# Optimization experiments

Measured on AMD Instinct MI355X. Metric: run time of the kernel, lower is better.

The kernel has to match this reference:

```python
import jax, jax.numpy as jnp
import numpy as np

N_NODES = 100000
N_EDGES = 3200000


def setup_inputs() -> dict:
    key = jax.random.key(0)
    k1, k2, k3, k4 = jax.random.split(key, 4)
    x = jax.random.normal(k1, (N_NODES, 16), dtype=jnp.float32)
    edge_index = jax.random.randint(k2, (2, N_EDGES), 0, N_NODES, dtype=jnp.int64)
    # Glorot-ish init like PyG's GCNConv linear layer
    W1 = jax.random.normal(k3, (16, 32), dtype=jnp.float32) * (1.0 / np.sqrt(16))
    b1 = jnp.zeros((32,), dtype=jnp.float32)
    W2 = jax.random.normal(k4, (32, 2), dtype=jnp.float32) * (1.0 / np.sqrt(32))
    b2 = jnp.zeros((2,), dtype=jnp.float32)
    return {"x": x, "edge_index": edge_index, "W1": W1, "b1": b1, "W2": W2, "b2": b2}


def _gcn_conv(x, W, b, src, dst, n):
    """PyG GCNConv: add self-loops, symmetric deg^{-1/2} normalization,
    linear transform, scatter-add aggregation, then bias."""
    h = x @ W  # [N, out]
    ones = jnp.ones(src.shape[0], dtype=x.dtype)
    deg = jax.ops.segment_sum(ones, dst, num_segments=n)  # in-degree incl. self-loops
    dinv = jnp.where(deg > 0, jax.lax.rsqrt(deg), 0.0)
    norm = dinv[src] * dinv[dst]  # [E+N]
    msg = h[src] * norm[:, None]  # gather + scale, [E+N, out]
    out = jax.ops.segment_sum(msg, dst, num_segments=n)  # scatter-add
    return out + b


def reference(x, edge_index, W1, b1, W2, b2):
    n = x.shape[0]
    loop = jnp.arange(n, dtype=edge_index.dtype)
    src = jnp.concatenate([edge_index[0], loop])  # self-loops appended
    dst = jnp.concatenate([edge_index[1], loop])
    h = jax.nn.relu(_gcn_conv(x, W1, b1, src, dst, n))
    return _gcn_conv(h, W2, b2, src, dst, n)
```

## Files before the change

### kernel.cpp

```cpp
#include <hip/hip_runtime.h>
#include <hip/hip_fp16.h>


#define B 256
#define NB_MAX 1024
#define BDIV 128
#define BSHIFT 7
#define CHUNK 4096
#define BCAP 6144
#define RI_MASK 0x7FFFFFu

__global__ __launch_bounds__(256) void k_phist(const int* __restrict__ dst,
                                               unsigned short* __restrict__ hists,
                                               int E, int NB, int NBLK) {
    __shared__ int h[NB_MAX];
    int tid = threadIdx.x, blk = blockIdx.x;
    for (int b = tid; b < NB; b += 256) h[b] = 0;
    __syncthreads();
    int start = blk * CHUNK;
    int end = min(start + CHUNK, E);
    for (int e = start + tid; e < end; e += 256)
        atomicAdd(&h[((unsigned)dst[e]) >> BSHIFT], 1);
    __syncthreads();
    for (int b = tid; b < NB; b += 256) hists[b * NBLK + blk] = (unsigned short)h[b];
}

__global__ __launch_bounds__(1024) void k_pscan1(unsigned short* __restrict__ hists,
                                                 int* __restrict__ totals, int NBLK) {
    __shared__ int s[1024];
    int b = blockIdx.x, tid = threadIdx.x;
    int v = (tid < NBLK) ? (int)hists[b * NBLK + tid] : 0;
    s[tid] = v;
    __syncthreads();
    for (int off = 1; off < 1024; off <<= 1) {
        int u = (tid >= off) ? s[tid - off] : 0;
        __syncthreads();
        s[tid] += u;
        __syncthreads();
    }
    if (tid < NBLK) hists[b * NBLK + tid] = (unsigned short)(s[tid] - v);
    if (tid == 1023) totals[b] = s[1023];
}

__global__ __launch_bounds__(256) void k_move(const int* __restrict__ src,
                                              const int* __restrict__ dst,
                                              const unsigned short* __restrict__ hists,
                                              const int* __restrict__ totals,
                                              unsigned* __restrict__ packed,
                                              int E, int NB, int NBLK) {
    __shared__ unsigned stage[CHUNK];
    __shared__ unsigned short stage_b[CHUNK];
    __shared__ int lh[NB_MAX];
    __shared__ int lexc[NB_MAX];
    __shared__ int gb[NB_MAX];
    __shared__ int part[256];
    int tid = threadIdx.x, blk = blockIdx.x;
    int t4 = tid * 4;
    {
        int a0 = (t4 + 0 < NB) ? totals[t4 + 0] : 0;
        int a1 = (t4 + 1 < NB) ? totals[t4 + 1] : 0;
        int a2 = (t4 + 2 < NB) ? totals[t4 + 2] : 0;
        int a3 = (t4 + 3 < NB) ? totals[t4 + 3] : 0;
        int sum = a0 + a1 + a2 + a3;
        part[tid] = sum;
        __syncthreads();
        for (int off = 1; off < 256; off <<= 1) {
            int u = (tid >= off) ? part[tid - off] : 0;
            __syncthreads();
            part[tid] += u;
            __syncthreads();
        }
        int run = part[tid] - sum;
        if (t4 + 0 < NB) { gb[t4 + 0] = run; run += a0; }
        if (t4 + 1 < NB) { gb[t4 + 1] = run; run += a1; }
        if (t4 + 2 < NB) { gb[t4 + 2] = run; run += a2; }
        if (t4 + 3 < NB) { gb[t4 + 3] = run; run += a3; }
    }
    for (int b = tid; b < NB; b += 256) lh[b] = 0;
    __syncthreads();
    int start = blk * CHUNK;
    int end = min(start + CHUNK, E);
    for (int e = start + tid; e < end; e += 256)
        atomicAdd(&lh[((unsigned)dst[e]) >> BSHIFT], 1);
    __syncthreads();
    {
        int a0 = 0, a1 = 0, a2 = 0, a3 = 0;
        if (t4 + 0 < NB) a0 = lh[t4 + 0];
        if (t4 + 1 < NB) a1 = lh[t4 + 1];
        if (t4 + 2 < NB) a2 = lh[t4 + 2];
        if (t4 + 3 < NB) a3 = lh[t4 + 3];
        int sum = a0 + a1 + a2 + a3;
        part[tid] = sum;
        __syncthreads();
        for (int off = 1; off < 256; off <<= 1) {
            int u = (tid >= off) ? part[tid - off] : 0;
            __syncthreads();
            part[tid] += u;
            __syncthreads();
        }
        int run = part[tid] - sum;
        if (t4 + 0 < NB) { lexc[t4 + 0] = run; run += a0; }
        if (t4 + 1 < NB) { lexc[t4 + 1] = run; run += a1; }
        if (t4 + 2 < NB) { lexc[t4 + 2] = run; run += a2; }
        if (t4 + 3 < NB) { lexc[t4 + 3] = run; run += a3; }
    }
    __syncthreads();
    for (int b = tid; b < NB; b += 256) {
        gb[b] = gb[b] + (int)hists[b * NBLK + blk] - lexc[b];
        lh[b] = lexc[b];
    }
    __syncthreads();
    for (int e = start + tid; e < end; e += 256) {
        unsigned d = (unsigned)dst[e];
        int b = d >> BSHIFT;
        int r = atomicAdd(&lh[b], 1);
        stage[r] = (unsigned)src[e] | ((d & (BDIV - 1u)) << 20);
        stage_b[r] = (unsigned short)b;
    }
    __syncthreads();
    int cnt = end - start;
    for (int i = tid; i < cnt; i += 256)
        packed[gb[stage_b[i]] + i] = stage[i];
}

__global__ __launch_bounds__(256) void k_bucket_csr(const unsigned* __restrict__ packed,
                                                    const int* __restrict__ totals,
                                                    unsigned* __restrict__ rowinfo,
                                                    float* __restrict__ dinv,
                                                    int* __restrict__ col, int n, int NB) {
    __shared__ unsigned stg[BCAP];
    __shared__ int part[256];
    __shared__ int lcnt[BDIV];
    __shared__ int plexc[BDIV];
    __shared__ int sbase[2];
    int b = blockIdx.x, tid = threadIdx.x;
    int t4 = tid * 4;
    {
        int a0 = (t4 + 0 < NB) ? totals[t4 + 0] : 0;
        int a1 = (t4 + 1 < NB) ? totals[t4 + 1] : 0;
        int a2 = (t4 + 2 < NB) ? totals[t4 + 2] : 0;
        int a3 = (t4 + 3 < NB) ? totals[t4 + 3] : 0;
        int sum = a0 + a1 + a2 + a3;
        part[tid] = sum;
        __syncthreads();
        for (int off = 1; off < 256; off <<= 1) {
            int u = (tid >= off) ? part[tid - off] : 0;
            __syncthreads();
            part[tid] += u;
            __syncthreads();
        }
        int run = part[tid] - sum;
        int a[4] = {a0, a1, a2, a3};
#pragma unroll
        for (int q = 0; q < 4; ++q) {
            if (t4 + q == b) { sbase[0] = run; sbase[1] = run + a[q]; }
            run += a[q];
        }
    }
    if (tid < BDIV) lcnt[tid] = 0;
    __syncthreads();
    int s0 = sbase[0], s1 = sbase[1];
    for (int i = s0 + tid; i < s1; i += 256) {
        unsigned u = packed[i];
        int k = i - s0;
        if (k < BCAP) stg[k] = u;
        atomicAdd(&lcnt[u >> 20], 1);
    }
    __syncthreads();
    int v = (tid < BDIV) ? lcnt[tid] : 0;
    int vp = (v + 7) & ~7;
    if (tid < BDIV) plexc[tid] = vp;
    __syncthreads();
    for (int off = 1; off < BDIV; off <<= 1) {
        int u = (tid < BDIV && tid >= off) ? plexc[tid - off] : 0;
        __syncthreads();
        if (tid < BDIV) plexc[tid] += u;
        __syncthreads();
    }
    int cb = s0 + 1024 * b;
    if (tid < BDIV) {
        plexc[tid] -= vp;
        int node = b * BDIV + tid;
        if (node < n) {
            rowinfo[node] = (unsigned)(cb + plexc[tid]) | ((unsigned)(vp >> 3) << 23);
            dinv[node] = rsqrtf((float)(v + 1));
        }
        lcnt[tid] = 0;
    }
    __syncthreads();
    for (int i = s0 + tid; i < s1; i += 256) {
        int k = i - s0;
        unsigned u = (k < BCAP) ? stg[k] : packed[i];
        int l = (int)(u >> 20);
        int pos = cb + plexc[l] + atomicAdd(&lcnt[l], 1);
        col[pos] = (int)(u & 0xFFFFFu);
    }
    __syncthreads();
    if (tid < BDIV) {
        int st = cb + plexc[tid];
        for (int k = v; k < vp; ++k) col[st + k] = n;
    }
}

__global__ void k_prep(const float* __restrict__ x, const float* __restrict__ dinv,
                       __half2* __restrict__ x16, float* __restrict__ t, int n8) {
    int g = blockIdx.x * blockDim.x + threadIdx.x;
    if (g < n8) {
        float d = dinv[g >> 3];
        float2 v = ((const float2*)x)[g];
        x16[g] = __float22half2_rn(make_float2(v.x * d, v.y * d));
    } else if (g < n8 + 8) {
        x16[g] = __float22half2_rn(make_float2(0.f, 0.f));
        if (g == n8) {
            t[(n8 >> 3) * 2 + 0] = 0.f;
            t[(n8 >> 3) * 2 + 1] = 0.f;
        }
    }
}

__global__ __launch_bounds__(256) void k_l1w(const __half2* __restrict__ x16,
                                             const unsigned* __restrict__ rowinfo,
                                             const int* __restrict__ col,
                                             const float* __restrict__ dinv,
                                             float* __restrict__ agg, int n) {
    int tid = threadIdx.x;
    int lane = tid & 63;
    int r = blockIdx.x * 4 + (tid >> 6);
    if (r >= n) return;
    int h = lane & 7, eg = lane >> 3;
    float dr = dinv[r];
    unsigned ri = rowinfo[r];
    int j = (int)(ri & RI_MASK) + eg;
    int trips = (int)(ri >> 23);
    float s0 = 0.f, s1 = 0.f;
    if (eg == 0) {
        float2 f = __half22float2(x16[(size_t)r * 8 + h]);
        s0 = f.x; s1 = f.y;
    }
#pragma unroll 4
    for (int it = 0; it < trips; ++it, j += 8) {
        int sc = col[j];
        float2 f = __half22float2(x16[(size_t)sc * 8 + h]);
        s0 += f.x; s1 += f.y;
    }
    s0 += __shfl_xor(s0, 8);  s1 += __shfl_xor(s1, 8);
    s0 += __shfl_xor(s0, 16); s1 += __shfl_xor(s1, 16);
    s0 += __shfl_xor(s0, 32); s1 += __shfl_xor(s1, 32);
    if (eg == 0)
        *(float2*)(agg + (size_t)r * 16 + 2 * h) = make_float2(s0 * dr, s1 * dr);
}

__global__ __launch_bounds__(256) void k_mlp(const float* __restrict__ agg,
                                             const float* __restrict__ dinv,
                                             const float* __restrict__ W1,
                                             const float* __restrict__ b1,
                                             const float* __restrict__ W2,
                                             float* __restrict__ t, int n) {
    __shared__ float sW1[512], sW2[64], sb1[32];
    int tid = threadIdx.x;
    for (int k = tid; k < 512; k += 256) sW1[k] = W1[k];
    if (tid < 64) sW2[tid] = W2[tid];
    if (tid < 32) sb1[tid] = b1[tid];
    __syncthreads();
    int i = blockIdx.x * 256 + tid;
    if (i >= n) return;
    float a[16];
    const float4* av = (const float4*)(agg + (size_t)i * 16);
#pragma unroll
    for (int q = 0; q < 4; ++q) {
        float4 v = av[q];
        a[4 * q + 0] = v.x; a[4 * q + 1] = v.y;
        a[4 * q + 2] = v.z; a[4 * q + 3] = v.w;
    }
    float di = dinv[i];
    float t0 = 0.f, t1 = 0.f;
#pragma unroll
    for (int j = 0; j < 32; ++j) {
        float acc = sb1[j];
#pragma unroll
        for (int k = 0; k < 16; ++k) acc = fmaf(a[k], sW1[k * 32 + j], acc);
        float hh = fmaxf(acc, 0.f);
        t0 = fmaf(hh, sW2[j * 2 + 0], t0);
        t1 = fmaf(hh, sW2[j * 2 + 1], t1);
    }
    t[(size_t)i * 2 + 0] = t0 * di;
    t[(size_t)i * 2 + 1] = t1 * di;
}

__global__ __launch_bounds__(256) void k_l2w(const unsigned* __restrict__ rowinfo,
                                             const int* __restrict__ col,
                                             const float* __restrict__ dinv,
                                             const float* __restrict__ ts,
                                             const float* __restrict__ b2,
                                             float* __restrict__ out, int n) {
    int g = blockIdx.x * 256 + threadIdx.x;
    int i = g >> 3, q = g & 7;
    if (i >= n) return;
    float di = dinv[i];
    unsigned ri = rowinfo[i];
    int j = (int)(ri & RI_MASK) + q;
    int trips = (int)(ri >> 23);
    float a0 = 0.f, a1 = 0.f;
    if (q == 0) {
        float2 tv = *(const float2*)(ts + (size_t)i * 2);
        a0 = tv.x; a1 = tv.y;
    }
#pragma unroll 4
    for (int it = 0; it < trips; ++it, j += 8) {
        int sc = col[j];
        float2 tv = *(const float2*)(ts + (size_t)sc * 2);
        a0 += tv.x; a1 += tv.y;
    }
    a0 += __shfl_xor(a0, 1); a1 += __shfl_xor(a1, 1);
    a0 += __shfl_xor(a0, 2); a1 += __shfl_xor(a1, 2);
    a0 += __shfl_xor(a0, 4); a1 += __shfl_xor(a1, 4);
    if (q == 0) {
        out[(size_t)i * 2 + 0] = fmaf(a0, di, b2[0]);
        out[(size_t)i * 2 + 1] = fmaf(a1, di, b2[1]);
    }
}


__global__ void k_zero(int* __restrict__ cnt, int n) {
    int i = blockIdx.x * blockDim.x + threadIdx.x;
    if (i < n) cnt[i] = 0;
}
__global__ void k_hist_rank(const int* __restrict__ dst, int* __restrict__ cnt,
                            int* __restrict__ rank, int E) {
    int e = blockIdx.x * blockDim.x + threadIdx.x;
    if (e < E) rank[e] = atomicAdd(&cnt[dst[e]], 1);
}
__global__ __launch_bounds__(256) void k_blocksum(const int* __restrict__ cnt,
                                                  int* __restrict__ bsum, int n) {
    __shared__ int s[256];
    int tid = threadIdx.x;
    int bse = blockIdx.x * 1024 + tid * 4;
    int sum = 0;
#pragma unroll
    for (int q = 0; q < 4; ++q) {
        int i = bse + q;
        if (i < n) sum += (cnt[i] + 7) & ~7;
    }
    s[tid] = sum;
    __syncthreads();
    for (int off = 128; off > 0; off >>= 1) {
        if (tid < off) s[tid] += s[tid + off];
        __syncthreads();
    }
    if (tid == 0) bsum[blockIdx.x] = s[0];
}
__global__ __launch_bounds__(1024) void k_scan_bsums(const int* __restrict__ bsum,
                                                     int* __restrict__ boff, int nb) {
    __shared__ int s[1024];
    int tid = threadIdx.x;
    int v = (tid < nb) ? bsum[tid] : 0;
    s[tid] = v;
    __syncthreads();
    for (int off = 1; off < 1024; off <<= 1) {
        int u = (tid >= off) ? s[tid - off] : 0;
        __syncthreads();
        s[tid] += u;
        __syncthreads();
    }
    if (tid < nb) boff[tid] = s[tid] - v;
}
__global__ __launch_bounds__(256) void k_scan_apply(const int* __restrict__ cnt,
                                                    const int* __restrict__ boff,
                                                    unsigned* __restrict__ rowinfo,
                                                    float* __restrict__ dinv, int n) {
    __shared__ int s[256];
    int tid = threadIdx.x;
    int bse = blockIdx.x * 1024 + tid * 4;
    int c[4];
    int sum = 0;
#pragma unroll
    for (int q = 0; q < 4; ++q) {
        int i = bse + q;
        c[q] = (i < n) ? ((cnt[i] + 7) & ~7) : 0;
        sum += c[q];
    }
    s[tid] = sum;
    __syncthreads();
    for (int off = 1; off < 256; off <<= 1) {
        int u = (tid >= off) ? s[tid - off] : 0;
        __syncthreads();
        s[tid] += u;
        __syncthreads();
    }
    int run = boff[blockIdx.x] + s[tid] - sum;
#pragma unroll
    for (int q = 0; q < 4; ++q) {
        int i = bse + q;
        if (i < n) {
            rowinfo[i] = (unsigned)run | ((unsigned)(c[q] >> 3) << 23);
            run += c[q];
            dinv[i] = rsqrtf((float)(cnt[i] + 1));
        }
    }
}
__global__ void k_fill_rank(const int* __restrict__ src, const int* __restrict__ dst,
                            const unsigned* __restrict__ rowinfo,
                            const int* __restrict__ rank,
                            int* __restrict__ col, int E) {
    int e = blockIdx.x * blockDim.x + threadIdx.x;
    if (e >= E) return;
    int d = dst[e];
    col[(rowinfo[d] & RI_MASK) + rank[e]] = src[e];
}
__global__ void k_pad_sent(const unsigned* __restrict__ rowinfo,
                           const int* __restrict__ cnt,
                           int* __restrict__ col, int n) {
    int i = blockIdx.x * blockDim.x + threadIdx.x;
    if (i >= n) return;
    int st = (int)(rowinfo[i] & RI_MASK);
    int v = cnt[i], vp = (v + 7) & ~7;
    for (int k = v; k < vp; ++k) col[st + k] = n;
}

static inline size_t align4(size_t v) { return (v + 3) & ~(size_t)3; }

extern "C" void kernel_launch(void* const* d_in, const int* in_sizes, int n_in,
                              void* d_out, int out_size, void* d_ws, size_t ws_size,
                              hipStream_t stream) {
    const float* x  = (const float*)d_in[0];
    const int*   ei = (const int*)d_in[1];
    const float* W1 = (const float*)d_in[2];
    const float* b1 = (const float*)d_in[3];
    const float* W2 = (const float*)d_in[4];
    const float* b2 = (const float*)d_in[5];
    float* out = (float*)d_out;

    const int n = in_sizes[0] / 16;
    const int E = in_sizes[1] / 2;
    const int* src = ei;
    const int* dst = ei + E;

    const int gn = (n + B - 1) / B;
    const int ge = (E + B - 1) / B;
    const int n8 = n * 8;

    const int NB   = (n + BDIV - 1) / BDIV;
    const int NBLK = (E + CHUNK - 1) / CHUNK;

    size_t o_hists  = 0;
    size_t o_totals = align4(o_hists + ((size_t)NB * NBLK + 1) / 2);
    size_t o_rowinf = align4(o_totals + NB);
    size_t o_dinv   = align4(o_rowinf + n);
    size_t o_packed = align4(o_dinv + n);
    size_t o_col    = align4(o_packed + E);
    size_t colsz    = (size_t)E + 1024 * (size_t)NB;
    size_t need_r5  = (o_col + colsz) * 4 + 64;
    size_t u_t   = 0;
    size_t u_x16 = align4(2 * (size_t)n + 2);
    size_t u_agg = align4(u_x16 + 8 * (size_t)n + 8);
    size_t reuse_need = u_agg + 16 * (size_t)n;

    bool r5_ok = (NB <= NB_MAX) && (NBLK <= 1024) && (n <= (1 << 20)) &&
                 ((size_t)E + 1024 * (size_t)NB < (RI_MASK + 1)) &&
                 (reuse_need <= (size_t)E) && (ws_size >= need_r5);

    if (r5_ok) {
        int* ws = (int*)d_ws;
        unsigned short* hists = (unsigned short*)(ws + o_hists);
        int*      totals = ws + o_totals;
        unsigned* rowinf = (unsigned*)(ws + o_rowinf);
        float*    dinv   = (float*)(ws + o_dinv);
        unsigned* packed = (unsigned*)(ws + o_packed);
        int*      col    = ws + o_col;
        float*    t      = (float*)(packed + u_t);
        __half2*  x16    = (__half2*)(packed + u_x16);
        float*    agg    = (float*)(packed + u_agg);

        k_phist<<<NBLK, 256, 0, stream>>>(dst, hists, E, NB, NBLK);
        k_pscan1<<<NB, 1024, 0, stream>>>(hists, totals, NBLK);
        k_move<<<NBLK, 256, 0, stream>>>(src, dst, hists, totals, packed, E, NB, NBLK);
        k_bucket_csr<<<NB, 256, 0, stream>>>(packed, totals, rowinf, dinv, col, n, NB);
        k_prep<<<(n8 + 8 + 255) / 256, 256, 0, stream>>>(x, dinv, x16, t, n8);
        k_l1w<<<(n + 3) / 4, 256, 0, stream>>>(x16, rowinf, col, dinv, agg, n);
        k_mlp<<<gn, 256, 0, stream>>>(agg, dinv, W1, b1, W2, t, n);
        k_l2w<<<(8 * n + 255) / 256, 256, 0, stream>>>(rowinf, col, dinv, t, b2, out, n);
        return;
    }

    const int nb = (n + 1023) / 1024;
    size_t f_cnt    = 0;
    size_t f_rowinf = align4(f_cnt + n);
    size_t f_col    = align4(f_rowinf + n);
    size_t f_dinv   = align4(f_col + E + 8 * (size_t)n);
    size_t f_bsum   = align4(f_dinv + n);
    size_t f_boff   = align4(f_bsum + nb);
    size_t f_rank   = align4(f_boff + nb);
    size_t reuse2   = align4(2 * (size_t)n + 2) + align4(8 * (size_t)n + 8) + 16 * (size_t)n;
    size_t rmax = (size_t)E > reuse2 ? (size_t)E : reuse2;
    size_t need_rank = (f_rank + rmax) * 4 + 64;
    if (ws_size >= need_rank && nb <= 1024) {
        int*      ws     = (int*)d_ws;
        int*      cnt    = ws + f_cnt;
        unsigned* rowinf = (unsigned*)(ws + f_rowinf);
        int*      col    = ws + f_col;
        float*    dinv   = (float*)(ws + f_dinv);
        int*      bsum   = ws + f_bsum;
        int*      boff   = ws + f_boff;
        int*      rank   = ws + f_rank;
        float*    t      = (float*)rank;
        __half2*  x16    = (__half2*)(rank + align4(2 * (size_t)n + 2));
        float*    agg    = (float*)(rank + align4(2 * (size_t)n + 2) + align4(8 * (size_t)n + 8));

        k_zero<<<gn, B, 0, stream>>>(cnt, n);
        k_hist_rank<<<ge, B, 0, stream>>>(dst, cnt, rank, E);
        k_blocksum<<<nb, 256, 0, stream>>>(cnt, bsum, n);
        k_scan_bsums<<<1, 1024, 0, stream>>>(bsum, boff, nb);
        k_scan_apply<<<nb, 256, 0, stream>>>(cnt, boff, rowinf, dinv, n);
        k_fill_rank<<<ge, B, 0, stream>>>(src, dst, rowinf, rank, col, E);
        k_pad_sent<<<gn, B, 0, stream>>>(rowinf, cnt, col, n);
        k_prep<<<(n8 + 8 + 255) / 256, 256, 0, stream>>>(x, dinv, x16, t, n8);
        k_l1w<<<(n + 3) / 4, 256, 0, stream>>>(x16, rowinf, col, dinv, agg, n);
        k_mlp<<<gn, 256, 0, stream>>>(agg, dinv, W1, b1, W2, t, n);
        k_l2w<<<(8 * n + 255) / 256, 256, 0, stream>>>(rowinf, col, dinv, t, b2, out, n);
    }
}
```

Baseline: 132.5 us.

## Transpose histogram layout and derive local counts from prefix scan in move kernel

The per-block bucket histogram is stored block-major instead of bucket-major, so the phist writes and the move kernel reads are coalesced. The move kernel no longer re-histograms its chunk of dst. It recovers each block's per-bucket counts as the difference between adjacent blocks' exclusive offsets (or the total for the last block), and fuses the two shared-memory scans into one pass. This removes a full read of dst plus atomics per block, at the cost of strided access in k_pscan1.

```diff
diff --git a/kernel.cpp b/kernel.cpp
--- a/kernel.cpp
+++ b/kernel.cpp
@@ -22,14 +22,16 @@
     for (int e = start + tid; e < end; e += 256)
         atomicAdd(&h[((unsigned)dst[e]) >> BSHIFT], 1);
     __syncthreads();
-    for (int b = tid; b < NB; b += 256) hists[b * NBLK + blk] = (unsigned short)h[b];
+    for (int b = tid; b < NB; b += 256)
+        hists[(size_t)blk * NB + b] = (unsigned short)h[b];
 }
 
 __global__ __launch_bounds__(1024) void k_pscan1(unsigned short* __restrict__ hists,
-                                                 int* __restrict__ totals, int NBLK) {
+                                                 int* __restrict__ totals,
+                                                 int NB, int NBLK) {
     __shared__ int s[1024];
     int b = blockIdx.x, tid = threadIdx.x;
-    int v = (tid < NBLK) ? (int)hists[b * NBLK + tid] : 0;
+    int v = (tid < NBLK) ? (int)hists[(size_t)tid * NB + b] : 0;
     s[tid] = v;
     __syncthreads();
     for (int off = 1; off < 1024; off <<= 1) {
@@ -38,7 +40,7 @@
         s[tid] += u;
         __syncthreads();
     }
-    if (tid < NBLK) hists[b * NBLK + tid] = (unsigned short)(s[tid] - v);
+    if (tid < NBLK) hists[(size_t)tid * NB + b] = (unsigned short)(s[tid] - v);
     if (tid == 1023) totals[b] = s[1023];
 }
 
@@ -53,63 +55,53 @@
     __shared__ int lh[NB_MAX];
     __shared__ int lexc[NB_MAX];
     __shared__ int gb[NB_MAX];
-    __shared__ int part[256];
+    __shared__ int partA[256];
+    __shared__ int partB[256];
     int tid = threadIdx.x, blk = blockIdx.x;
     int t4 = tid * 4;
-    {
-        int a0 = (t4 + 0 < NB) ? totals[t4 + 0] : 0;
-        int a1 = (t4 + 1 < NB) ? totals[t4 + 1] : 0;
-        int a2 = (t4 + 2 < NB) ? totals[t4 + 2] : 0;
-        int a3 = (t4 + 3 < NB) ? totals[t4 + 3] : 0;
-        int sum = a0 + a1 + a2 + a3;
-        part[tid] = sum;
-        __syncthreads();
-        for (int off = 1; off < 256; off <<= 1) {
-            int u = (tid >= off) ? part[tid - off] : 0;
-            __syncthreads();
-            part[tid] += u;
-            __syncthreads();
-        }
-        int run = part[tid] - sum;
-        if (t4 + 0 < NB) { gb[t4 + 0] = run; run += a0; }
-        if (t4 + 1 < NB) { gb[t4 + 1] = run; run += a1; }
-        if (t4 + 2 < NB) { gb[t4 + 2] = run; run += a2; }
-        if (t4 + 3 < NB) { gb[t4 + 3] = run; run += a3; }
-    }
-    for (int b = tid; b < NB; b += 256) lh[b] = 0;
+    bool last = (blk == NBLK - 1);
+    int a[4], c[4], myoff[4];
+    int sumA = 0, sumB = 0;
+#pragma unroll
+    for (int q = 0; q < 4; ++q) {
+        int b = t4 + q;
+        int tA = 0, mo = 0, cc = 0;
+        if (b < NB) {
+            tA = totals[b];
+            mo = (int)hists[(size_t)blk * NB + b];
+            int nxt = last ? tA : (int)hists[(size_t)(blk + 1) * NB + b];
+            cc = nxt - mo;
+        }
+        a[q] = tA; myoff[q] = mo; c[q] = cc;
+        sumA += tA; sumB += cc;
+    }
+    partA[tid] = sumA;
+    partB[tid] = sumB;
+    __syncthreads();
+    for (int off = 1; off < 256; off <<= 1) {
+        int uA = (tid >= off) ? partA[tid - off] : 0;
+        int uB = (tid >= off) ? partB[tid - off] : 0;
+        __syncthreads();
+        partA[tid] += uA;
+        partB[tid] += uB;
+        __syncthreads();
+    }
+    int runA = partA[tid] - sumA;
+    int runB = partB[tid] - sumB;
+#pragma unroll
+    for (int q = 0; q < 4; ++q) {
+        int b = t4 + q;
+        if (b < NB) {
+            gb[b] = runA + myoff[q] - runB;
+            lexc[b] = runB;
+            lh[b] = runB;
+        }
+        runA += a[q];
+        runB += c[q];
+    }
     __syncthreads();
     int start = blk * CHUNK;
     int end = min(start + CHUNK, E);
-    for (int e = start + tid; e < end; e += 256)
-        atomicAdd(&lh[((unsigned)dst[e]) >> BSHIFT], 1);
-    __syncthreads();
-    {
-        int a0 = 0, a1 = 0, a2 = 0, a3 = 0;
-        if (t4 + 0 < NB) a0 = lh[t4 + 0];
-        if (t4 + 1 < NB) a1 = lh[t4 + 1];
-        if (t4 + 2 < NB) a2 = lh[t4 + 2];
-        if (t4 + 3 < NB) a3 = lh[t4 + 3];
-        int sum = a0 + a1 + a2 + a3;
-        part[tid] = sum;
-        __syncthreads();
-        for (int off = 1; off < 256; off <<= 1) {
-            int u = (tid >= off) ? part[tid - off] : 0;
-            __syncthreads();
-            part[tid] += u;
-            __syncthreads();
-        }
-        int run = part[tid] - sum;
-        if (t4 + 0 < NB) { lexc[t4 + 0] = run; run += a0; }
-        if (t4 + 1 < NB) { lexc[t4 + 1] = run; run += a1; }
-        if (t4 + 2 < NB) { lexc[t4 + 2] = run; run += a2; }
-        if (t4 + 3 < NB) { lexc[t4 + 3] = run; run += a3; }
-    }
-    __syncthreads();
-    for (int b = tid; b < NB; b += 256) {
-        gb[b] = gb[b] + (int)hists[b * NBLK + blk] - lexc[b];
-        lh[b] = lexc[b];
-    }
-    __syncthreads();
     for (int e = start + tid; e < end; e += 256) {
         unsigned d = (unsigned)dst[e];
         int b = d >> BSHIFT;
@@ -472,7 +464,7 @@
         float*    agg    = (float*)(packed + u_agg);
 
         k_phist<<<NBLK, 256, 0, stream>>>(dst, hists, E, NB, NBLK);
-        k_pscan1<<<NB, 1024, 0, stream>>>(hists, totals, NBLK);
+        k_pscan1<<<NB, 1024, 0, stream>>>(hists, totals, NB, NBLK);
         k_move<<<NBLK, 256, 0, stream>>>(src, dst, hists, totals, packed, E, NB, NBLK);
         k_bucket_csr<<<NB, 256, 0, stream>>>(packed, totals, rowinf, dinv, col, n, NB);
         k_prep<<<(n8 + 8 + 255) / 256, 256, 0, stream>>>(x, dinv, x16, t, n8);
```

Measured after the change: 130.1 us. About the same (-1.8%).
